# Optimization experiments

Measured on AMD Instinct MI355X. Metric: run time of the kernel, lower is better.

Reference implementation:

```python
import jax, jax.numpy as jnp
import numpy as np

EPS = 1e-5
R = 3


def _layernorm(x, gamma, beta):
    mu = jnp.mean(x, axis=-1, keepdims=True)
    var = jnp.mean(jnp.square(x - mu), axis=-1, keepdims=True)
    return (x - mu) * jax.lax.rsqrt(var + EPS) * gamma + beta


def setup_inputs() -> dict:
    key = jax.random.key(0)
    ks = jax.random.split(key, 16)
    N, C, H, W = 32, 256, 32, 32
    ic = C // 2
    L = H * W
    R2 = R * R
    d_attn = R2 * L        # 9216
    d_out = ic * L         # 131072
    return {
        "x": jax.random.normal(ks[0], (N, C, H, W), jnp.float32),
        "wq": jax.random.normal(ks[1], (ic, C), jnp.float32) / np.sqrt(C),
        "wk": jax.random.normal(ks[2], (ic, C), jnp.float32) / np.sqrt(C),
        "gamma1": jnp.ones((d_attn,), jnp.float32),
        "beta1": jnp.zeros((d_attn,), jnp.float32),
        "w1": jax.random.normal(ks[3], (C, d_attn), jnp.float32) / np.sqrt(d_attn),
        "b1": jnp.zeros((C,), jnp.float32),
        "w2": jax.random.normal(ks[4], (d_out, C), jnp.float32) / np.sqrt(C),
        "b2": jnp.zeros((d_out,), jnp.float32),
        "gamma2": jnp.ones((d_out,), jnp.float32),
        "beta2": jnp.zeros((d_out,), jnp.float32),
        "w_out": jax.random.normal(ks[5], (C, ic), jnp.float32) / np.sqrt(ic),
        "bn_gamma": jax.random.normal(ks[6], (C,), jnp.float32),
        "bn_beta": jax.random.normal(ks[7], (C,), jnp.float32),
        "bn_mean": jax.random.normal(ks[8], (C,), jnp.float32),
        "bn_var": jax.random.uniform(ks[9], (C,), jnp.float32, 0.5, 1.5),
    }


def reference(x, wq, wk, gamma1, beta1, w1, b1, w2, b2, gamma2, beta2,
              w_out, bn_gamma, bn_beta, bn_mean, bn_var):
    N, C, H, W = x.shape
    ic = wq.shape[0]
    L = H * W
    R2 = R * R
    pad = (R - 1) // 2

    # 1x1 convs == channel GEMMs
    q = jnp.einsum('nchw,oc->nohw', x, wq).reshape(N, ic, L)       # [N,ic,L]
    k = jnp.einsum('nchw,oc->nohw', x, wk)                          # [N,ic,H,W]

    # unfold: RxR local patches, torch channel-major ordering [ic, R2]
    kp = jnp.pad(k, ((0, 0), (0, 0), (pad, pad), (pad, pad)))
    patches = jnp.stack([kp[:, :, i:i + H, j:j + W]
                         for i in range(R) for j in range(R)], axis=-1)
    patches = patches.reshape(N, ic, L, R2)                         # [N,ic,L,R2]

    # local attention scores: q . k over channels at each spatial loc
    f = jnp.einsum('ncl,nclr->nlr', q, patches)                     # [N,L,R2]
    f = f.transpose(0, 2, 1).reshape(N, R2 * L)                     # [N, R2*L]

    # f = f + dropout(f) -> identity at inference => 2f
    f = f + f
    f = _layernorm(f, gamma1, beta1)

    # FFN
    h = jax.nn.relu(f @ w1.T + b1)                                  # [N,C]
    h = h @ w2.T + b2                                               # [N, ic*L]
    h = _layernorm(h, gamma2, beta2)
    y = h.reshape(N, ic, H, W)

    # output 1x1 conv + BatchNorm2d (inference mode)
    wy = jnp.einsum('nchw,oc->nohw', y, w_out)                      # [N,C,H,W]
    scale = (bn_gamma * jax.lax.rsqrt(bn_var + EPS))[None, :, None, None]
    wy = (wy - bn_mean[None, :, None, None]) * scale + bn_beta[None, :, None, None]
    return wy + x
```

## Files before the change

### kernel.cpp

```cpp
#include <hip/hip_runtime.h>

#define NN 32
#define CC 256
#define LL 1024
#define IC 128
#define DA 9216
#define DOUT 131072
#define EPSF 1e-5f

typedef __attribute__((ext_vector_type(8))) short short8;
typedef __attribute__((ext_vector_type(4))) float f32x4;

__device__ __forceinline__ ushort bf_rne(float f) {
  union { float f; unsigned u; } v;
  v.f = f;
  unsigned u = v.u;
  u += 0x7FFF + ((u >> 16) & 1);
  return (ushort)(u >> 16);
}

__device__ __forceinline__ unsigned bfp2(float lo, float hi) {
  union { float f; unsigned u; } a, b;
  a.f = lo; b.f = hi;
  return __builtin_amdgcn_perm(b.u + 0x8000u, a.u + 0x8000u, 0x07060302u);
}

__global__ __launch_bounds__(256) void k_wcvt(const float* __restrict__ wq,
                                              const float* __restrict__ wk,
                                              const float* __restrict__ wo,
                                              ushort* __restrict__ wqkbf,
                                              ushort* __restrict__ wobf,
                                              float* __restrict__ fz) {
  int b = blockIdx.x;
  if (b < 96) {
    int idx = (b * 256 + threadIdx.x) * 4;
    float4 v;
    if (idx < 32768) v = *(const float4*)(wq + idx);
    else if (idx < 65536) v = *(const float4*)(wk + idx - 32768);
    else v = *(const float4*)(wo + idx - 65536);
    uint2 o;
    o.x = bfp2(v.x, v.y);
    o.y = bfp2(v.z, v.w);
    if (idx < 65536) *(uint2*)(wqkbf + idx) = o;
    else *(uint2*)(wobf + idx - 65536) = o;
  } else {
    int idx = ((b - 96) * 256 + threadIdx.x) * 4;
    if (idx < 294976)
      *(float4*)(fz + idx) = make_float4(0.f, 0.f, 0.f, 0.f);
  }
}

__global__ __launch_bounds__(256, 4) void k_qkx(const float* __restrict__ x,
                                                const ushort* __restrict__ wqkbf,
                                                float* __restrict__ q,
                                                float* __restrict__ k) {
  __shared__ ushort xl[64 * 264];
  int t = threadIdx.x;
  int n = blockIdx.y;
  int l0 = blockIdx.x * 64;
  int lane = t & 63, wv = t >> 6;
  int m16 = lane & 15, kg = lane >> 4;

  {
    int l = t & 63, g = t >> 6;
    const float* xn = x + ((size_t)n * CC) * LL + l0 + l;
#pragma unroll
    for (int i = 0; i < 8; i++) {
      int c8 = (i * 4 + g) * 8;
      float v[8];
#pragma unroll
      for (int j = 0; j < 8; j++) v[j] = xn[(size_t)(c8 + j) * LL];
      union { short8 s; unsigned u[4]; } p;
      p.u[0] = bfp2(v[0], v[1]);
      p.u[1] = bfp2(v[2], v[3]);
      p.u[2] = bfp2(v[4], v[5]);
      p.u[3] = bfp2(v[6], v[7]);
      *(short8*)&xl[l * 264 + c8] = p.s;
    }
  }
  __syncthreads();

  f32x4 acc[2][2][4];
#pragma unroll
  for (int mt = 0; mt < 2; mt++)
#pragma unroll
    for (int ms = 0; ms < 2; ms++)
#pragma unroll
      for (int ls = 0; ls < 4; ls++) acc[mt][ms][ls] = (f32x4){0.f, 0.f, 0.f, 0.f};

#pragma unroll
  for (int kc = 0; kc < 8; kc++) {
    short8 a[2][2];
#pragma unroll
    for (int mt = 0; mt < 2; mt++)
#pragma unroll
      for (int ms = 0; ms < 2; ms++)
        a[mt][ms] = *(const short8*)(wqkbf +
            (((mt * 128 + wv * 32 + ms * 16 + m16) << 8) + kc * 32 + kg * 8));
#pragma unroll
    for (int ls = 0; ls < 4; ls++) {
      short8 b = *(const short8*)&xl[(ls * 16 + m16) * 264 + kc * 32 + kg * 8];
      acc[0][0][ls] =
          __builtin_amdgcn_mfma_f32_16x16x32_bf16(a[0][0], b, acc[0][0][ls], 0, 0, 0);
      acc[0][1][ls] =
          __builtin_amdgcn_mfma_f32_16x16x32_bf16(a[0][1], b, acc[0][1][ls], 0, 0, 0);
      acc[1][0][ls] =
          __builtin_amdgcn_mfma_f32_16x16x32_bf16(a[1][0], b, acc[1][0][ls], 0, 0, 0);
      acc[1][1][ls] =
          __builtin_amdgcn_mfma_f32_16x16x32_bf16(a[1][1], b, acc[1][1][ls], 0, 0, 0);
    }
  }

#pragma unroll
  for (int mt = 0; mt < 2; mt++) {
    float* outp = (mt ? k : q) + (size_t)n * IC * LL;
#pragma unroll
    for (int ms = 0; ms < 2; ms++)
#pragma unroll
      for (int ls = 0; ls < 4; ls++) {
        int col = l0 + ls * 16 + m16;
#pragma unroll
        for (int r = 0; r < 4; r++)
          outp[(size_t)(wv * 32 + ms * 16 + kg * 4 + r) * LL + col] =
              acc[mt][ms][ls][r];
      }
  }
}

__global__ __launch_bounds__(256) void k_attn(const float* __restrict__ q,
                                              const float* __restrict__ k,
                                              float* __restrict__ f2) {
  int n = blockIdx.x;
  int c0 = blockIdx.y * 32;
  int l = blockIdx.z * 256 + threadIdx.x;
  int h = l >> 5, w = l & 31;
  const float* qn = q + (size_t)n * IC * LL;
  const float* kn = k + (size_t)n * IC * LL;
  bool val[9];
  int off[9];
#pragma unroll
  for (int i = 0; i < 3; i++)
#pragma unroll
    for (int j = 0; j < 3; j++) {
      int r = i * 3 + j;
      int hh = h + i - 1, ww = w + j - 1;
      val[r] = (hh >= 0 && hh < 32 && ww >= 0 && ww < 32);
      off[r] = hh * 32 + ww;
    }
  float acc[9];
#pragma unroll
  for (int r = 0; r < 9; r++) acc[r] = 0.f;
#pragma unroll 4
  for (int cc = 0; cc < 32; cc++) {
    int c = c0 + cc;
    float qv = qn[c * LL + l];
    const float* kc = kn + c * LL;
#pragma unroll
    for (int r = 0; r < 9; r++) {
      float kv = val[r] ? kc[off[r]] : 0.f;
      acc[r] += qv * kv;
    }
  }
#pragma unroll
  for (int r = 0; r < 9; r++)
    atomicAdd(&f2[(size_t)n * DA + r * LL + l], 2.f * acc[r]);
}

__global__ __launch_bounds__(256) void k_ln1(float* __restrict__ f2,
                                             const float* __restrict__ g1,
                                             const float* __restrict__ b1) {
  int n = blockIdx.x, t = threadIdx.x;
  float* row = f2 + (size_t)n * DA;
  float4 v[9];
  float s = 0.f, ss = 0.f;
#pragma unroll
  for (int kk = 0; kk < 9; kk++) {
    v[kk] = ((const float4*)row)[t + kk * 256];
    s += v[kk].x + v[kk].y + v[kk].z + v[kk].w;
    ss += v[kk].x * v[kk].x + v[kk].y * v[kk].y + v[kk].z * v[kk].z +
          v[kk].w * v[kk].w;
  }
#pragma unroll
  for (int o = 32; o; o >>= 1) {
    s += __shfl_down(s, o);
    ss += __shfl_down(ss, o);
  }
  __shared__ float ps[4], pss[4], stats[2];
  int wid = t >> 6, lid = t & 63;
  if (lid == 0) { ps[wid] = s; pss[wid] = ss; }
  __syncthreads();
  if (t == 0) {
    float S = ps[0] + ps[1] + ps[2] + ps[3];
    float SS = pss[0] + pss[1] + pss[2] + pss[3];
    float mu = S / DA;
    float var = SS / DA - mu * mu;
    stats[0] = mu;
    stats[1] = rsqrtf(var + EPSF);
  }
  __syncthreads();
  float mu = stats[0], rs = stats[1];
#pragma unroll
  for (int kk = 0; kk < 9; kk++) {
    float4 g = ((const float4*)g1)[t + kk * 256];
    float4 b = ((const float4*)b1)[t + kk * 256];
    float4 o;
    o.x = (v[kk].x - mu) * rs * g.x + b.x;
    o.y = (v[kk].y - mu) * rs * g.y + b.y;
    o.z = (v[kk].z - mu) * rs * g.z + b.z;
    o.w = (v[kk].w - mu) * rs * g.w + b.w;
    ((float4*)row)[t + kk * 256] = o;
  }
}

__global__ __launch_bounds__(256) void k_ffn1(const float* __restrict__ fln,
                                              const float* __restrict__ w1,
                                              const float* __restrict__ b1,
                                              ushort* __restrict__ h1bf) {
  int o = blockIdx.x, nsb = blockIdx.y * 16, t = threadIdx.x;
  float acc[16];
#pragma unroll
  for (int i = 0; i < 16; i++) acc[i] = 0.f;
  const float4* w1r = (const float4*)(w1 + (size_t)o * DA);
  for (int kk = 0; kk < 9; kk++) {
    float4 wv = w1r[t + kk * 256];
#pragma unroll
    for (int i = 0; i < 16; i++) {
      float4 fv = ((const float4*)(fln + (size_t)(nsb + i) * DA))[t + kk * 256];
      acc[i] += wv.x * fv.x + wv.y * fv.y + wv.z * fv.z + wv.w * fv.w;
    }
  }
#pragma unroll
  for (int i = 0; i < 16; i++)
#pragma unroll
    for (int s = 32; s; s >>= 1) acc[i] += __shfl_down(acc[i], s);
  __shared__ float part[4][16];
  int wid = t >> 6, lid = t & 63;
  if (lid == 0) {
#pragma unroll
    for (int i = 0; i < 16; i++) part[wid][i] = acc[i];
  }
  __syncthreads();
  if (t < 16) {
    float sum = part[0][t] + part[1][t] + part[2][t] + part[3][t] + b1[o];
    h1bf[(size_t)(nsb + t) * CC + o] = bf_rne(fmaxf(sum, 0.f));
  }
}

__global__ __launch_bounds__(256, 2) void k_ffn2(
    const ushort* __restrict__ h1bf, const float* __restrict__ w2,
    const float* __restrict__ b2, float* __restrict__ h2,
    float* __restrict__ st) {
  __shared__ ushort wt[128 * 264];
  __shared__ float bs[64];
  int t = threadIdx.x;
  int j0 = blockIdx.x * 128;
  if (t < 64) bs[t] = 0.f;

  {
    const float* wsrc = w2 + (size_t)j0 * CC;
    int row_t = t >> 6;
    int col_t = (t & 63) * 4;
#pragma unroll
    for (int io = 0; io < 4; io++) {
      float4 v[8];
#pragma unroll
      for (int u = 0; u < 8; u++)
        v[u] = *(const float4*)(wsrc + (size_t)(io * 8 + u) * 1024 + t * 4);
#pragma unroll
      for (int u = 0; u < 8; u++) {
        int row = (io * 8 + u) * 4 + row_t;
        uint2 p;
        p.x = bfp2(v[u].x, v[u].y);
        p.y = bfp2(v[u].z, v[u].w);
        *(uint2*)&wt[row * 264 + col_t] = p;
      }
    }
  }
  __syncthreads();

  int lane = t & 63, wv = t >> 6;
  int m16 = lane & 15, kg = lane >> 4;
  int jw = j0 + wv * 32;
  int j[2] = {jw + m16, jw + 16 + m16};

  f32x4 acc[2][2];
#pragma unroll
  for (int m = 0; m < 2; m++)
#pragma unroll
    for (int nn = 0; nn < 2; nn++) acc[m][nn] = (f32x4){0.f, 0.f, 0.f, 0.f};

#pragma unroll
  for (int kc = 0; kc < 8; kc++) {
    short8 a0 = *(const short8*)(h1bf + m16 * CC + kc * 32 + kg * 8);
    short8 a1 = *(const short8*)(h1bf + (16 + m16) * CC + kc * 32 + kg * 8);
#pragma unroll
    for (int nn = 0; nn < 2; nn++) {
      short8 b = *(const short8*)&wt[(wv * 32 + nn * 16 + m16) * 264 +
                                     kc * 32 + kg * 8];
      acc[0][nn] =
          __builtin_amdgcn_mfma_f32_16x16x32_bf16(a0, b, acc[0][nn], 0, 0, 0);
      acc[1][nn] =
          __builtin_amdgcn_mfma_f32_16x16x32_bf16(a1, b, acc[1][nn], 0, 0, 0);
    }
  }

  float b2v[2] = {b2[j[0]], b2[j[1]]};

  float s8[2][4], q8[2][4];
#pragma unroll
  for (int m = 0; m < 2; m++)
#pragma unroll
    for (int r = 0; r < 4; r++) { s8[m][r] = 0.f; q8[m][r] = 0.f; }
#pragma unroll
  for (int m = 0; m < 2; m++)
#pragma unroll
    for (int nn = 0; nn < 2; nn++) {
#pragma unroll
      for (int r = 0; r < 4; r++) {
        float v = acc[m][nn][r] + b2v[nn];
        int row = m * 16 + kg * 4 + r;
        h2[(size_t)row * DOUT + j[nn]] = v;
        s8[m][r] += v;
        q8[m][r] += v * v;
      }
    }
#pragma unroll
  for (int off = 8; off; off >>= 1)
#pragma unroll
    for (int m = 0; m < 2; m++)
#pragma unroll
      for (int r = 0; r < 4; r++) {
        s8[m][r] += __shfl_down(s8[m][r], off, 16);
        q8[m][r] += __shfl_down(q8[m][r], off, 16);
      }
  if (m16 == 0) {
#pragma unroll
    for (int m = 0; m < 2; m++)
#pragma unroll
      for (int r = 0; r < 4; r++) {
        int row = m * 16 + kg * 4 + r;
        atomicAdd(&bs[row], s8[m][r]);
        atomicAdd(&bs[32 + row], q8[m][r]);
      }
  }
  __syncthreads();
  if (t < 64) atomicAdd(&st[t], bs[t]);
}

__global__ __launch_bounds__(256, 4) void k_out(
    const float* __restrict__ h2, const float* __restrict__ st,
    const float* __restrict__ g2, const float* __restrict__ b2,
    const ushort* __restrict__ wobf, const float* __restrict__ bn_g,
    const float* __restrict__ bn_b, const float* __restrict__ bn_m,
    const float* __restrict__ bn_v, const float* __restrict__ x,
    float* __restrict__ out) {
  __shared__ ushort yl[32 * 136];
  int t = threadIdx.x;
  int n = blockIdx.y;
  int l0 = blockIdx.x * 32;
  float mu = st[n] * (1.f / DOUT);
  float rs = rsqrtf(st[32 + n] * (1.f / DOUT) - mu * mu + EPSF);

  {
    int l = t & 31, og = t >> 5;
    const float* h2n = h2 + (size_t)n * DOUT;
#pragma unroll
    for (int half = 0; half < 2; half++) {
      float y[8];
#pragma unroll
      for (int jj = 0; jj < 8; jj++) {
        int o = og * 16 + half * 8 + jj;
        int d = o * LL + l0 + l;
        y[jj] = (h2n[d] - mu) * rs * g2[d] + b2[d];
      }
      union { short8 s; unsigned u[4]; } p;
      p.u[0] = bfp2(y[0], y[1]);
      p.u[1] = bfp2(y[2], y[3]);
      p.u[2] = bfp2(y[4], y[5]);
      p.u[3] = bfp2(y[6], y[7]);
      *(short8*)&yl[l * 136 + og * 16 + half * 8] = p.s;
    }
  }
  __syncthreads();

  int lane = t & 63, wv = t >> 6;
  int m16 = lane & 15, kg = lane >> 4;
  f32x4 acc[4][2];
#pragma unroll
  for (int ms = 0; ms < 4; ms++)
#pragma unroll
    for (int ls = 0; ls < 2; ls++) acc[ms][ls] = (f32x4){0.f, 0.f, 0.f, 0.f};

#pragma unroll
  for (int kc = 0; kc < 4; kc++) {
    short8 b[2];
#pragma unroll
    for (int ls = 0; ls < 2; ls++)
      b[ls] = *(const short8*)&yl[(ls * 16 + m16) * 136 + kc * 32 + kg * 8];
#pragma unroll
    for (int ms = 0; ms < 4; ms++) {
      short8 a = *(const short8*)(wobf +
          (((wv * 64 + ms * 16 + m16) << 7) + kc * 32 + kg * 8));
#pragma unroll
      for (int ls = 0; ls < 2; ls++)
        acc[ms][ls] =
            __builtin_amdgcn_mfma_f32_16x16x32_bf16(a, b[ls], acc[ms][ls], 0, 0, 0);
    }
  }

#pragma unroll
  for (int ms = 0; ms < 4; ms++)
#pragma unroll
    for (int r = 0; r < 4; r++) {
      int O = wv * 64 + ms * 16 + kg * 4 + r;
      float sc = bn_g[O] * rsqrtf(bn_v[O] + EPSF);
      float sh = bn_b[O] - bn_m[O] * sc;
#pragma unroll
      for (int ls = 0; ls < 2; ls++) {
        int col = l0 + ls * 16 + m16;
        size_t base = ((size_t)(n * CC + O)) * LL + col;
        out[base] = acc[ms][ls][r] * sc + sh + x[base];
      }
    }
}

extern "C" void kernel_launch(void* const* d_in, const int* in_sizes, int n_in,
                              void* d_out, int out_size, void* d_ws,
                              size_t ws_size, hipStream_t stream) {
  const float* x = (const float*)d_in[0];
  const float* wq = (const float*)d_in[1];
  const float* wk = (const float*)d_in[2];
  const float* gamma1 = (const float*)d_in[3];
  const float* beta1 = (const float*)d_in[4];
  const float* w1 = (const float*)d_in[5];
  const float* b1 = (const float*)d_in[6];
  const float* w2 = (const float*)d_in[7];
  const float* b2 = (const float*)d_in[8];
  const float* gamma2 = (const float*)d_in[9];
  const float* beta2 = (const float*)d_in[10];
  const float* w_out = (const float*)d_in[11];
  const float* bn_g = (const float*)d_in[12];
  const float* bn_b = (const float*)d_in[13];
  const float* bn_m = (const float*)d_in[14];
  const float* bn_v = (const float*)d_in[15];
  float* outp = (float*)d_out;
  float* ws = (float*)d_ws;

  float* qb = ws;
  float* kb = ws + 4194304;
  float* fb = ws + 8388608;
  float* stb = ws + 8683520;
  ushort* h1bfb = (ushort*)(ws + 8683584);
  ushort* wqkbfb = (ushort*)(ws + 8687680);
  ushort* wobfb = (ushort*)(ws + 8720448);
  float* h2b = qb;

  if (ws_size < 8736832ull * sizeof(float)) return;

  k_wcvt<<<dim3(385), 256, 0, stream>>>(wq, wk, w_out, wqkbfb, wobfb, fb);
  k_qkx<<<dim3(16, 32), 256, 0, stream>>>(x, wqkbfb, qb, kb);
  k_attn<<<dim3(32, 4, 4), 256, 0, stream>>>(qb, kb, fb);
  k_ln1<<<dim3(32), 256, 0, stream>>>(fb, gamma1, beta1);
  k_ffn1<<<dim3(256, 2), 256, 0, stream>>>(fb, w1, b1, h1bfb);
  k_ffn2<<<dim3(1024), 256, 0, stream>>>(h1bfb, w2, b2, h2b, stb);
  k_out<<<dim3(32, 32), 256, 0, stream>>>(h2b, stb, gamma2, beta2, wobfb,
                                          bn_g, bn_b, bn_m, bn_v, x, outp);
}
```

Baseline: 343.1 us.

## Use bf16 intermediates for FFN1 and h2; replace attention atomics with partial buffers

The attention kernel now writes per-channel-block partial scores into separate buffers, which LayerNorm1 sums. This replaces the atomicAdd accumulation and the zero-fill pass. LayerNorm1 writes bf16 output, w1 is converted to bf16 in the weight-conversion kernel, and FFN1 reads both operands as bf16. FFN2 stores h2 as bf16 to halve traffic in the output kernel, and its w2 staging loads all 32 rows at once. The w1 conversion adds a full read of w1 on every call, and bf16 storage of h2 and of the LN1 output adds rounding error.

Result: faster. 336.2 us (-2.0%).

```diff
diff --git a/kernel.cpp b/kernel.cpp
--- a/kernel.cpp
+++ b/kernel.cpp
@@ -19,6 +19,12 @@
   return (ushort)(u >> 16);
 }
 
+__device__ __forceinline__ float bf2f(ushort u) {
+  union { float f; unsigned v; } x;
+  x.v = ((unsigned)u) << 16;
+  return x.f;
+}
+
 __device__ __forceinline__ unsigned bfp2(float lo, float hi) {
   union { float f; unsigned u; } a, b;
   a.f = lo; b.f = hi;
@@ -28,9 +34,11 @@
 __global__ __launch_bounds__(256) void k_wcvt(const float* __restrict__ wq,
                                               const float* __restrict__ wk,
                                               const float* __restrict__ wo,
+                                              const float* __restrict__ w1,
                                               ushort* __restrict__ wqkbf,
                                               ushort* __restrict__ wobf,
-                                              float* __restrict__ fz) {
+                                              ushort* __restrict__ w1bf,
+                                              float* __restrict__ st) {
   int b = blockIdx.x;
   if (b < 96) {
     int idx = (b * 256 + threadIdx.x) * 4;
@@ -43,10 +51,15 @@
     o.y = bfp2(v.z, v.w);
     if (idx < 65536) *(uint2*)(wqkbf + idx) = o;
     else *(uint2*)(wobf + idx - 65536) = o;
+  } else if (b < 2400) {
+    int idx = ((b - 96) * 256 + threadIdx.x) * 4;
+    float4 v = *(const float4*)(w1 + idx);
+    uint2 o;
+    o.x = bfp2(v.x, v.y);
+    o.y = bfp2(v.z, v.w);
+    *(uint2*)(w1bf + idx) = o;
   } else {
-    int idx = ((b - 96) * 256 + threadIdx.x) * 4;
-    if (idx < 294976)
-      *(float4*)(fz + idx) = make_float4(0.f, 0.f, 0.f, 0.f);
+    if (threadIdx.x < 64) st[threadIdx.x] = 0.f;
   }
 }
 
@@ -129,9 +142,10 @@
 
 __global__ __launch_bounds__(256) void k_attn(const float* __restrict__ q,
                                               const float* __restrict__ k,
-                                              float* __restrict__ f2) {
+                                              float* __restrict__ f_part) {
   int n = blockIdx.x;
-  int c0 = blockIdx.y * 32;
+  int c0b = blockIdx.y;
+  int c0 = c0b * 32;
   int l = blockIdx.z * 256 + threadIdx.x;
   int h = l >> 5, w = l & 31;
   const float* qn = q + (size_t)n * IC * LL;
@@ -161,24 +175,33 @@
       acc[r] += qv * kv;
     }
   }
-#pragma unroll
-  for (int r = 0; r < 9; r++)
-    atomicAdd(&f2[(size_t)n * DA + r * LL + l], 2.f * acc[r]);
-}
-
-__global__ __launch_bounds__(256) void k_ln1(float* __restrict__ f2,
+  float* dst = f_part + ((size_t)(c0b * 32 + n)) * DA;
+#pragma unroll
+  for (int r = 0; r < 9; r++) dst[r * LL + l] = 2.f * acc[r];
+}
+
+__global__ __launch_bounds__(256) void k_ln1(const float* __restrict__ f_part,
                                              const float* __restrict__ g1,
-                                             const float* __restrict__ b1) {
+                                             const float* __restrict__ b1,
+                                             ushort* __restrict__ flnbf) {
   int n = blockIdx.x, t = threadIdx.x;
-  float* row = f2 + (size_t)n * DA;
   float4 v[9];
   float s = 0.f, ss = 0.f;
 #pragma unroll
   for (int kk = 0; kk < 9; kk++) {
-    v[kk] = ((const float4*)row)[t + kk * 256];
-    s += v[kk].x + v[kk].y + v[kk].z + v[kk].w;
-    ss += v[kk].x * v[kk].x + v[kk].y * v[kk].y + v[kk].z * v[kk].z +
-          v[kk].w * v[kk].w;
+    int e4 = t + kk * 256;
+    float4 a = ((const float4*)(f_part + ((size_t)(0 * 32 + n)) * DA))[e4];
+    float4 b = ((const float4*)(f_part + ((size_t)(1 * 32 + n)) * DA))[e4];
+    float4 c = ((const float4*)(f_part + ((size_t)(2 * 32 + n)) * DA))[e4];
+    float4 d = ((const float4*)(f_part + ((size_t)(3 * 32 + n)) * DA))[e4];
+    float4 o;
+    o.x = a.x + b.x + c.x + d.x;
+    o.y = a.y + b.y + c.y + d.y;
+    o.z = a.z + b.z + c.z + d.z;
+    o.w = a.w + b.w + c.w + d.w;
+    v[kk] = o;
+    s += o.x + o.y + o.z + o.w;
+    ss += o.x * o.x + o.y * o.y + o.z * o.z + o.w * o.w;
   }
 #pragma unroll
   for (int o = 32; o; o >>= 1) {
@@ -199,34 +222,42 @@
   }
   __syncthreads();
   float mu = stats[0], rs = stats[1];
+  ushort* fln = flnbf + (size_t)n * DA;
 #pragma unroll
   for (int kk = 0; kk < 9; kk++) {
-    float4 g = ((const float4*)g1)[t + kk * 256];
-    float4 b = ((const float4*)b1)[t + kk * 256];
+    int e4 = t + kk * 256;
+    float4 g = ((const float4*)g1)[e4];
+    float4 b = ((const float4*)b1)[e4];
     float4 o;
     o.x = (v[kk].x - mu) * rs * g.x + b.x;
     o.y = (v[kk].y - mu) * rs * g.y + b.y;
     o.z = (v[kk].z - mu) * rs * g.z + b.z;
     o.w = (v[kk].w - mu) * rs * g.w + b.w;
-    ((float4*)row)[t + kk * 256] = o;
-  }
-}
-
-__global__ __launch_bounds__(256) void k_ffn1(const float* __restrict__ fln,
-                                              const float* __restrict__ w1,
+    uint2 p;
+    p.x = bfp2(o.x, o.y);
+    p.y = bfp2(o.z, o.w);
+    *(uint2*)(fln + e4 * 4) = p;
+  }
+}
+
+__global__ __launch_bounds__(256) void k_ffn1(const ushort* __restrict__ flnbf,
+                                              const ushort* __restrict__ w1bf,
                                               const float* __restrict__ b1,
                                               ushort* __restrict__ h1bf) {
   int o = blockIdx.x, nsb = blockIdx.y * 16, t = threadIdx.x;
   float acc[16];
 #pragma unroll
   for (int i = 0; i < 16; i++) acc[i] = 0.f;
-  const float4* w1r = (const float4*)(w1 + (size_t)o * DA);
+  const ushort* w1r = w1bf + (size_t)o * DA;
   for (int kk = 0; kk < 9; kk++) {
-    float4 wv = w1r[t + kk * 256];
+    int e = kk * 1024 + t * 4;
+    ushort4 wu = *(const ushort4*)(w1r + e);
+    float w0 = bf2f(wu.x), w1v = bf2f(wu.y), w2v = bf2f(wu.z), w3 = bf2f(wu.w);
 #pragma unroll
     for (int i = 0; i < 16; i++) {
-      float4 fv = ((const float4*)(fln + (size_t)(nsb + i) * DA))[t + kk * 256];
-      acc[i] += wv.x * fv.x + wv.y * fv.y + wv.z * fv.z + wv.w * fv.w;
+      ushort4 fu = *(const ushort4*)(flnbf + (size_t)(nsb + i) * DA + e);
+      acc[i] += w0 * bf2f(fu.x) + w1v * bf2f(fu.y) + w2v * bf2f(fu.z) +
+                w3 * bf2f(fu.w);
     }
   }
 #pragma unroll
@@ -248,7 +279,7 @@
 
 __global__ __launch_bounds__(256, 2) void k_ffn2(
     const ushort* __restrict__ h1bf, const float* __restrict__ w2,
-    const float* __restrict__ b2, float* __restrict__ h2,
+    const float* __restrict__ b2, ushort* __restrict__ h2u,
     float* __restrict__ st) {
   __shared__ ushort wt[128 * 264];
   __shared__ float bs[64];
@@ -260,20 +291,17 @@
     const float* wsrc = w2 + (size_t)j0 * CC;
     int row_t = t >> 6;
     int col_t = (t & 63) * 4;
-#pragma unroll
-    for (int io = 0; io < 4; io++) {
-      float4 v[8];
-#pragma unroll
-      for (int u = 0; u < 8; u++)
-        v[u] = *(const float4*)(wsrc + (size_t)(io * 8 + u) * 1024 + t * 4);
-#pragma unroll
-      for (int u = 0; u < 8; u++) {
-        int row = (io * 8 + u) * 4 + row_t;
-        uint2 p;
-        p.x = bfp2(v[u].x, v[u].y);
-        p.y = bfp2(v[u].z, v[u].w);
-        *(uint2*)&wt[row * 264 + col_t] = p;
-      }
+    float4 v[32];
+#pragma unroll
+    for (int u = 0; u < 32; u++)
+      v[u] = *(const float4*)(wsrc + (size_t)u * 1024 + t * 4);
+#pragma unroll
+    for (int u = 0; u < 32; u++) {
+      int row = u * 4 + row_t;
+      uint2 p;
+      p.x = bfp2(v[u].x, v[u].y);
+      p.y = bfp2(v[u].z, v[u].w);
+      *(uint2*)&wt[row * 264 + col_t] = p;
     }
   }
   __syncthreads();
@@ -319,7 +347,7 @@
       for (int r = 0; r < 4; r++) {
         float v = acc[m][nn][r] + b2v[nn];
         int row = m * 16 + kg * 4 + r;
-        h2[(size_t)row * DOUT + j[nn]] = v;
+        h2u[(size_t)row * DOUT + j[nn]] = bf_rne(v);
         s8[m][r] += v;
         q8[m][r] += v * v;
       }
@@ -348,7 +376,7 @@
 }
 
 __global__ __launch_bounds__(256, 4) void k_out(
-    const float* __restrict__ h2, const float* __restrict__ st,
+    const ushort* __restrict__ h2u, const float* __restrict__ st,
     const float* __restrict__ g2, const float* __restrict__ b2,
     const ushort* __restrict__ wobf, const float* __restrict__ bn_g,
     const float* __restrict__ bn_b, const float* __restrict__ bn_m,
@@ -363,7 +391,7 @@
 
   {
     int l = t & 31, og = t >> 5;
-    const float* h2n = h2 + (size_t)n * DOUT;
+    const ushort* h2n = h2u + (size_t)n * DOUT;
 #pragma unroll
     for (int half = 0; half < 2; half++) {
       float y[8];
@@ -371,7 +399,7 @@
       for (int jj = 0; jj < 8; jj++) {
         int o = og * 16 + half * 8 + jj;
         int d = o * LL + l0 + l;
-        y[jj] = (h2n[d] - mu) * rs * g2[d] + b2[d];
+        y[jj] = (bf2f(h2n[d]) - mu) * rs * g2[d] + b2[d];
       }
       union { short8 s; unsigned u[4]; } p;
       p.u[0] = bfp2(y[0], y[1]);
@@ -448,21 +476,24 @@
 
   float* qb = ws;
   float* kb = ws + 4194304;
-  float* fb = ws + 8388608;
-  float* stb = ws + 8683520;
-  ushort* h1bfb = (ushort*)(ws + 8683584);
-  ushort* wqkbfb = (ushort*)(ws + 8687680);
-  ushort* wobfb = (ushort*)(ws + 8720448);
-  float* h2b = qb;
-
-  if (ws_size < 8736832ull * sizeof(float)) return;
-
-  k_wcvt<<<dim3(385), 256, 0, stream>>>(wq, wk, w_out, wqkbfb, wobfb, fb);
+  float* fpart = ws + 8388608;
+  float* stb = ws + 9568256;
+  ushort* h1bfb = (ushort*)(ws + 9568320);
+  ushort* flnbfb = (ushort*)(ws + 9572416);
+  ushort* wqkbfb = (ushort*)(ws + 9719872);
+  ushort* wobfb = (ushort*)(ws + 9752640);
+  ushort* w1bfb = (ushort*)(ws + 9769024);
+  ushort* h2ub = (ushort*)qb;
+
+  if (ws_size < 10948672ull * sizeof(float)) return;
+
+  k_wcvt<<<dim3(2401), 256, 0, stream>>>(wq, wk, w_out, w1, wqkbfb, wobfb,
+                                         w1bfb, stb);
   k_qkx<<<dim3(16, 32), 256, 0, stream>>>(x, wqkbfb, qb, kb);
-  k_attn<<<dim3(32, 4, 4), 256, 0, stream>>>(qb, kb, fb);
-  k_ln1<<<dim3(32), 256, 0, stream>>>(fb, gamma1, beta1);
-  k_ffn1<<<dim3(256, 2), 256, 0, stream>>>(fb, w1, b1, h1bfb);
-  k_ffn2<<<dim3(1024), 256, 0, stream>>>(h1bfb, w2, b2, h2b, stb);
-  k_out<<<dim3(32, 32), 256, 0, stream>>>(h2b, stb, gamma2, beta2, wobfb,
+  k_attn<<<dim3(32, 4, 4), 256, 0, stream>>>(qb, kb, fpart);
+  k_ln1<<<dim3(32), 256, 0, stream>>>(fpart, gamma1, beta1, flnbfb);
+  k_ffn1<<<dim3(256, 2), 256, 0, stream>>>(flnbfb, w1bfb, b1, h1bfb);
+  k_ffn2<<<dim3(1024), 256, 0, stream>>>(h1bfb, w2, b2, h2ub, stb);
+  k_out<<<dim3(32, 32), 256, 0, stream>>>(h2ub, stb, gamma2, beta2, wobfb,
                                           bn_g, bn_b, bn_m, bn_v, x, outp);
 }
```
